# Kernel optimization log

Measured on AMD Instinct MI355X. Metric: run time of the kernel, lower is better.

Reference implementation:

```python
import jax, jax.numpy as jnp
import numpy as np

EPS = 0.1
P, C, T_MLP, C_MLP, B = 196, 768, 384, 3072, 64


def yat(x, W, b, alpha):
    # x: (..., in), W: (out, in), b: (out,), alpha: (1,)
    dot_nb = jnp.einsum('...i,oi->...o', x, W)          # no-bias dot (shared GEMM)
    dot = dot_nb + b
    w_norm_sq = jnp.sum(W * W, axis=1)                   # (out,)
    x_norm_sq = jnp.sum(x * x, axis=-1, keepdims=True)   # (..., 1)
    dist_sq = w_norm_sq + x_norm_sq - 2.0 * dot_nb
    out_f = W.shape[0]
    scale_base = out_f / np.log(out_f + 1.0)
    scale = jnp.sqrt(jnp.asarray(scale_base, x.dtype)) ** alpha[0]
    return scale * (dot * dot) / (dist_sq + EPS)


def setup_inputs() -> dict:
    key = jax.random.key(0)
    ks = jax.random.split(key, 7)
    x = jax.random.normal(ks[0], (B, P, C), dtype=jnp.float32)
    # token-mixing YAT: in=P, out=T_MLP
    tw = jax.random.normal(ks[1], (T_MLP, P), dtype=jnp.float32) / np.sqrt(P)
    tb = jnp.zeros((T_MLP,), jnp.float32)
    t_alpha = jnp.ones((1,), jnp.float32)
    # token-mixing linear: T_MLP -> P
    w2 = jax.random.uniform(ks[2], (P, T_MLP), jnp.float32, -1, 1) / np.sqrt(T_MLP)
    b2 = jax.random.uniform(ks[3], (P,), jnp.float32, -1, 1) / np.sqrt(T_MLP)
    # channel-mixing YAT: in=C, out=C_MLP
    cw = jax.random.normal(ks[4], (C_MLP, C), dtype=jnp.float32) / np.sqrt(C)
    cb = jnp.zeros((C_MLP,), jnp.float32)
    c_alpha = jnp.ones((1,), jnp.float32)
    # channel-mixing linear: C_MLP -> C
    w4 = jax.random.uniform(ks[5], (C, C_MLP), jnp.float32, -1, 1) / np.sqrt(C_MLP)
    b4 = jax.random.uniform(ks[6], (C,), jnp.float32, -1, 1) / np.sqrt(C_MLP)
    return {"x": x, "tw": tw, "tb": tb, "t_alpha": t_alpha, "w2": w2, "b2": b2,
            "cw": cw, "cb": cb, "c_alpha": c_alpha, "w4": w4, "b4": b4}


def reference(x, tw, tb, t_alpha, w2, b2, cw, cb, c_alpha, w4, b4):
    # Token mixing (operates over patch dim)
    shortcut = x
    xt = jnp.swapaxes(x, 1, 2)                 # (B, C, P)
    h = yat(xt, tw, tb, t_alpha)               # (B, C, T_MLP)
    h = jnp.einsum('bct,pt->bcp', h, w2) + b2  # (B, C, P)
    x = shortcut + jnp.swapaxes(h, 1, 2)
    # Channel mixing (operates over hidden dim)
    shortcut = x
    h = yat(x, cw, cb, c_alpha)                # (B, P, C_MLP)
    h = jnp.einsum('bpm,cm->bpc', h, w4) + b4  # (B, P, C)
    return shortcut + h
```

## Files before the change

### kernel.cpp

```cpp
#include <hip/hip_runtime.h>
#include <hip/hip_bf16.h>
#include <math.h>

#define B_   64
#define P_   196
#define PPAD 224
#define C_   768
#define TM_  384
#define CM_  3072
#define EPSY 0.1f

typedef unsigned short u16;
typedef __attribute__((ext_vector_type(8))) short bf16x8;
typedef __attribute__((ext_vector_type(4))) float f32x4;

__device__ __forceinline__ float bf2f(u16 v) {
    return __uint_as_float(((unsigned int)v) << 16);
}
__device__ __forceinline__ u16 f2bf(float f) {
    unsigned int u = __float_as_uint(f);
    unsigned int rounding = 0x7FFFu + ((u >> 16) & 1u);
    return (u16)((u + rounding) >> 16);
}

__device__ __forceinline__ void gl_lds16(const u16* g, u16* l) {
    __builtin_amdgcn_global_load_lds(
        (const __attribute__((address_space(1))) unsigned int*)g,
        (__attribute__((address_space(3))) unsigned int*)l,
        16, 0, 0);
}


__global__ __launch_bounds__(256) void k_prep_xT(const float* __restrict__ x,
                                                 u16* __restrict__ xT,
                                                 float* __restrict__ xn1) {
    __shared__ u16 tile[32][33];
    __shared__ float colsum[32];
    const int b = blockIdx.z, p0 = blockIdx.x * 32, c0 = blockIdx.y * 32;
    const int tx = threadIdx.x & 31, ty = threadIdx.x >> 5;
    if (threadIdx.x < 32) colsum[threadIdx.x] = 0.f;
    const float* xb = x + (size_t)b * P_ * C_;
    float s = 0.f;
    #pragma unroll
    for (int r = 0; r < 4; ++r) {
        int p = p0 + ty + r * 8;
        float v = (p < P_) ? xb[(size_t)p * C_ + c0 + tx] : 0.f;
        u16 h = f2bf(v);
        tile[ty + r * 8][tx] = h;
        float vb = bf2f(h);
        s = fmaf(vb, vb, s);
    }
    __syncthreads();
    u16* dst = xT + ((size_t)b * C_ + c0) * PPAD + p0;
    #pragma unroll
    for (int r = 0; r < 4; ++r) {
        int cl = ty + r * 8;
        dst[(size_t)cl * PPAD + tx] = tile[tx][cl];
    }
    atomicAdd(&colsum[tx], s);
    __syncthreads();
    if (threadIdx.x < 32)
        atomicAdd(&xn1[(size_t)b * C_ + c0 + threadIdx.x], colsum[threadIdx.x]);
}

__device__ __forceinline__ void pad_norm_body(const float* in, u16* outb, float* norm,
                                              int rows, int inlen, int outlen,
                                              int bid, int tid) {
    int wave = (bid * 256 + tid) >> 6;
    int lane = tid & 63;
    if (wave >= rows) return;
    const float* src = in + (size_t)wave * inlen;
    u16* dst = outb + (size_t)wave * outlen;
    float s = 0.f;
    for (int i = lane; i < outlen; i += 64) {
        float v = (i < inlen) ? src[i] : 0.f;
        u16 h = f2bf(v);
        dst[i] = h;
        float vv = bf2f(h);
        s = fmaf(vv, vv, s);
    }
    #pragma unroll
    for (int off = 32; off > 0; off >>= 1) s += __shfl_down(s, off, 64);
    if (lane == 0) norm[wave] = s;
}

__global__ __launch_bounds__(256) void k_prep_weights(
    const float* __restrict__ tw, u16* __restrict__ twb, float* __restrict__ twn,
    const float* __restrict__ cw, u16* __restrict__ cwb, float* __restrict__ cwn,
    const float* __restrict__ w2, u16* __restrict__ w2b,
    const float* __restrict__ w4, u16* __restrict__ w4b) {
    int bid = blockIdx.x, tid = threadIdx.x;
    if (bid < 96) {
        pad_norm_body(tw, twb, twn, TM_, P_, PPAD, bid, tid);
    } else if (bid < 864) {
        pad_norm_body(cw, cwb, cwn, CM_, C_, C_, bid - 96, tid);
    } else if (bid < 1248) {
        int idx = (bid - 864) * 256 + tid;
        int row = idx / TM_;
        w2b[idx] = (row < P_) ? f2bf(w2[(size_t)row * TM_ + (idx % TM_)]) : (u16)0;
    } else {
        int idx = (bid - 1248) * 256 + tid;
        float4 v = ((const float4*)w4)[idx];
        ushort4 o;
        o.x = f2bf(v.x); o.y = f2bf(v.y); o.z = f2bf(v.z); o.w = f2bf(v.w);
        ((ushort4*)w4b)[idx] = o;
    }
}

__device__ __forceinline__ void mfma_mainloop(
    const u16* __restrict__ A, const u16* __restrict__ B,
    int lda, int ldb, int kiters,
    f32x4 (&acc)[4][4], u16* As, u16* Bs) {
    const int t = threadIdx.x;
    const int w = t >> 6, l = t & 63;
    const int quad = l >> 4, l15 = l & 15;
    const int row0 = t >> 2, kc = (t & 3) * 8;

    const u16* pa0 = A + (size_t)row0 * lda + kc;
    const u16* pa1 = A + (size_t)(64 + row0) * lda + kc;
    const u16* pb0 = B + (size_t)row0 * ldb + kc;
    const u16* pb1 = B + (size_t)(64 + row0) * ldb + kc;

    u16* ldsA0 = As + w * 512;
    u16* ldsA1 = As + 2048 + w * 512;
    u16* ldsB0 = Bs + w * 512;
    u16* ldsB1 = Bs + 2048 + w * 512;

#define STAGE_(bsel, koff)                          \
    do {                                            \
        const int nb_ = (bsel) * 4096;              \
        gl_lds16(pa0 + (koff), ldsA0 + nb_);        \
        gl_lds16(pa1 + (koff), ldsA1 + nb_);        \
        gl_lds16(pb0 + (koff), ldsB0 + nb_);        \
        gl_lds16(pb1 + (koff), ldsB1 + nb_);        \
    } while (0)

    STAGE_(0, 0);
    if (kiters > 1) {
        STAGE_(1, 32);
        asm volatile("s_waitcnt vmcnt(4)" ::: "memory");
    } else {
        asm volatile("s_waitcnt vmcnt(0)" ::: "memory");
    }
    __builtin_amdgcn_s_barrier();

    int cur = 0;
    int koff = 64;
    for (int it = 0; it < kiters; ++it) {
        const u16* Aw = As + cur * 4096 + (w >> 1) * 2048;
        const u16* Bw = Bs + cur * 4096 + (w & 1) * 2048;
        bf16x8 af[4], bfr[4];
        #pragma unroll
        for (int i = 0; i < 4; ++i)
            af[i] = *(const bf16x8*)(Aw + ((i * 16 + l15) * 32 + quad * 8));
        #pragma unroll
        for (int j = 0; j < 4; ++j)
            bfr[j] = *(const bf16x8*)(Bw + ((j * 16 + l15) * 32 + quad * 8));
        asm volatile("s_waitcnt lgkmcnt(0)" ::: "memory");
        __builtin_amdgcn_sched_barrier(0);
        __builtin_amdgcn_s_barrier();
        const bool more2 = (it + 2 < kiters);
        if (more2) { STAGE_(cur, koff); koff += 32; }
        __builtin_amdgcn_s_setprio(1);
        #pragma unroll
        for (int i = 0; i < 4; ++i)
            #pragma unroll
            for (int j = 0; j < 4; ++j)
                acc[i][j] = __builtin_amdgcn_mfma_f32_16x16x32_bf16(af[i], bfr[j], acc[i][j], 0, 0, 0);
        __builtin_amdgcn_s_setprio(0);
        if (it + 1 < kiters) {
            if (more2) asm volatile("s_waitcnt vmcnt(4)" ::: "memory");
            else       asm volatile("s_waitcnt vmcnt(0)" ::: "memory");
            __builtin_amdgcn_s_barrier();
        }
        cur ^= 1;
    }
#undef STAGE_
}

#define MFMA_CORE(AP, BP, LDA, LDB, KITERS)                              \
    __shared__ u16 As[2 * 128 * 32];                                     \
    __shared__ u16 Bs[2 * 128 * 32];                                     \
    const int t = threadIdx.x;                                           \
    const int wid = t >> 6, lane = t & 63;                               \
    const int quad = lane >> 4, l15 = lane & 15;                         \
    f32x4 acc[4][4];                                                     \
    _Pragma("unroll")                                                    \
    for (int i = 0; i < 4; ++i)                                          \
        _Pragma("unroll")                                                \
        for (int j = 0; j < 4; ++j) acc[i][j] = (f32x4){0.f,0.f,0.f,0.f};\
    mfma_mainloop(AP, BP, LDA, LDB, KITERS, acc, As, Bs);                \
    const int rbase = m0 + (wid >> 1) * 64;                              \
    const int cbase = n0 + (wid & 1) * 64;

__global__ __launch_bounds__(256) void k1_token_yat(
    const u16* __restrict__ xT, const u16* __restrict__ twb,
    const float* __restrict__ tb, const float* __restrict__ twn,
    const float* __restrict__ xn1, const float* __restrict__ alpha, float sb,
    u16* __restrict__ h1) {
    const int m0 = (blockIdx.x + blockIdx.y * 8) * 128;
    const int n0 = blockIdx.z * 128;
    MFMA_CORE(xT + (size_t)m0 * PPAD, twb + (size_t)n0 * PPAD, PPAD, PPAD, PPAD / 32)
    float scale = powf(sqrtf(sb), alpha[0]);
    #pragma unroll
    for (int i = 0; i < 4; ++i) {
        #pragma unroll
        for (int j = 0; j < 4; ++j) {
            int col = cbase + j * 16 + l15;
            float bn = tb[col], wnn = twn[col];
            #pragma unroll
            for (int reg = 0; reg < 4; ++reg) {
                int row = rbase + i * 16 + quad * 4 + reg;
                float dnb = acc[i][j][reg];
                float dot = dnb + bn;
                float dist = wnn + xn1[row] - 2.f * dnb;
                h1[(size_t)row * TM_ + col] = f2bf(scale * dot * dot / (dist + EPSY));
            }
        }
    }
}

__global__ __launch_bounds__(256) void k3_chan_yat(
    const u16* __restrict__ x1b, const u16* __restrict__ cwb,
    const float* __restrict__ cb, const float* __restrict__ cwn,
    const float* __restrict__ xn2, const float* __restrict__ alpha, float sb,
    u16* __restrict__ h3) {
    const int mt = blockIdx.x + blockIdx.y * 8;
    if (mt >= B_ * P_ / 128) return;
    const int m0 = mt * 128;
    const int n0 = blockIdx.z * 128;
    MFMA_CORE(x1b + (size_t)m0 * C_, cwb + (size_t)n0 * C_, C_, C_, C_ / 32)
    float scale = powf(sqrtf(sb), alpha[0]);
    #pragma unroll
    for (int i = 0; i < 4; ++i) {
        #pragma unroll
        for (int j = 0; j < 4; ++j) {
            int col = cbase + j * 16 + l15;
            float bn = cb[col], wnn = cwn[col];
            #pragma unroll
            for (int reg = 0; reg < 4; ++reg) {
                int row = rbase + i * 16 + quad * 4 + reg;
                float dnb = acc[i][j][reg];
                float dot = dnb + bn;
                float dist = wnn + xn2[row] - 2.f * dnb;
                h3[(size_t)row * CM_ + col] = f2bf(scale * dot * dot / (dist + EPSY));
            }
        }
    }
}

__global__ __launch_bounds__(256) void k2_token_out(
    const u16* __restrict__ w2b, const u16* __restrict__ h1,
    const float* __restrict__ b2, const float* __restrict__ x,
    float* __restrict__ xn2, u16* __restrict__ x1b) {
    const int m0 = blockIdx.x * 128, n0 = blockIdx.y * 128;
    const u16* Bz = h1 + (size_t)blockIdx.z * C_ * TM_;
    MFMA_CORE(w2b + (size_t)m0 * TM_, Bz + (size_t)n0 * TM_, TM_, TM_, TM_ / 32)
    const float* rz = x + (size_t)blockIdx.z * P_ * C_;
    u16* oz = x1b + (size_t)blockIdx.z * P_ * C_;
    float* xrow = xn2 + (size_t)blockIdx.z * P_;
    #pragma unroll
    for (int i = 0; i < 4; ++i) {
        #pragma unroll
        for (int reg = 0; reg < 4; ++reg) {
            int row = rbase + i * 16 + quad * 4 + reg;
            if (row < P_) {
                float bm = b2[row];
                float s = 0.f;
                #pragma unroll
                for (int j = 0; j < 4; ++j) {
                    int col = cbase + j * 16 + l15;
                    float v = acc[i][j][reg] + bm + rz[(size_t)row * C_ + col];
                    u16 h = f2bf(v);
                    oz[(size_t)row * C_ + col] = h;
                    float vb = bf2f(h);
                    s = fmaf(vb, vb, s);
                }
                s += __shfl_xor(s, 1, 64);
                s += __shfl_xor(s, 2, 64);
                s += __shfl_xor(s, 4, 64);
                s += __shfl_xor(s, 8, 64);
                if (l15 == 0) atomicAdd(&xrow[row], s);
            }
        }
    }
}

__global__ __launch_bounds__(256) void k4_split(
    const u16* __restrict__ h3, const u16* __restrict__ w4b,
    u16* __restrict__ pbuf, int KK) {
    const int mt = blockIdx.x + blockIdx.y * 8;
    if (mt >= B_ * P_ / 128) return;
    const int m0 = mt * 128;
    const int nz = blockIdx.z;
    const int n0 = (nz % (C_ / 128)) * 128;
    const int ks = nz / (C_ / 128);
    const int kbase = ks * KK;
    MFMA_CORE(h3 + (size_t)m0 * CM_ + kbase, w4b + (size_t)n0 * CM_ + kbase,
              CM_, CM_, KK / 32)
    u16* dst = pbuf + (size_t)ks * ((size_t)B_ * P_ * C_);
    #pragma unroll
    for (int i = 0; i < 4; ++i) {
        #pragma unroll
        for (int j = 0; j < 4; ++j) {
            int col = cbase + j * 16 + l15;
            #pragma unroll
            for (int reg = 0; reg < 4; ++reg) {
                int row = rbase + i * 16 + quad * 4 + reg;
                dst[(size_t)row * C_ + col] = f2bf(acc[i][j][reg]);
            }
        }
    }
}

template <int NS>
__global__ __launch_bounds__(256) void k4_reduce(
    float* __restrict__ outp, const u16* __restrict__ pbuf,
    const u16* __restrict__ x1b, const float* __restrict__ b4) {
    int idx = blockIdx.x * 256 + threadIdx.x;
    int c = (idx * 4) % C_;
    ushort4 r = ((const ushort4*)x1b)[idx];
    float4 o;
    o.x = bf2f(r.x) + b4[c + 0];
    o.y = bf2f(r.y) + b4[c + 1];
    o.z = bf2f(r.z) + b4[c + 2];
    o.w = bf2f(r.w) + b4[c + 3];
    const size_t stride4 = (size_t)B_ * P_ * C_ / 4;
    #pragma unroll
    for (int s = 0; s < NS; ++s) {
        ushort4 p = ((const ushort4*)pbuf)[idx + s * stride4];
        o.x += bf2f(p.x); o.y += bf2f(p.y); o.z += bf2f(p.z); o.w += bf2f(p.w);
    }
    ((float4*)outp)[idx] = o;
}

__global__ __launch_bounds__(256) void gemm_k4_fb(
    const u16* __restrict__ A, const u16* __restrict__ Bmat,
    const float* __restrict__ biasN, const u16* __restrict__ resB,
    float* __restrict__ Fout) {
    __shared__ u16 As[128 * 32];
    __shared__ u16 Bs[64 * 32];
    const int t = threadIdx.x;
    const int wid = t >> 6, lane = t & 63;
    const int quad = lane >> 4, l15 = lane & 15;
    const int m0 = blockIdx.x * 128, n0 = blockIdx.y * 64;
    f32x4 acc[4][2];
    #pragma unroll
    for (int i = 0; i < 4; ++i)
        #pragma unroll
        for (int j = 0; j < 2; ++j) acc[i][j] = (f32x4){0.f, 0.f, 0.f, 0.f};
    const u16* Aw = As + (wid >> 1) * (64 * 32);
    const u16* Bw = Bs + (wid & 1) * (32 * 32);
    const int arow = t >> 2, akc = (t & 3) * 8;
    for (int k0 = 0; k0 < CM_; k0 += 32) {
        gl_lds16(A + (size_t)(m0 + arow) * CM_ + k0 + akc,      As + wid * 512);
        gl_lds16(A + (size_t)(m0 + 64 + arow) * CM_ + k0 + akc, As + 2048 + wid * 512);
        gl_lds16(Bmat + (size_t)(n0 + arow) * CM_ + k0 + akc,   Bs + wid * 512);
        __syncthreads();
        bf16x8 af[4], bfr[2];
        #pragma unroll
        for (int i = 0; i < 4; ++i)
            af[i] = *(const bf16x8*)(Aw + ((i * 16 + l15) * 32 + quad * 8));
        #pragma unroll
        for (int j = 0; j < 2; ++j)
            bfr[j] = *(const bf16x8*)(Bw + ((j * 16 + l15) * 32 + quad * 8));
        #pragma unroll
        for (int i = 0; i < 4; ++i)
            #pragma unroll
            for (int j = 0; j < 2; ++j)
                acc[i][j] = __builtin_amdgcn_mfma_f32_16x16x32_bf16(af[i], bfr[j], acc[i][j], 0, 0, 0);
        __syncthreads();
    }
    const int rbase = m0 + (wid >> 1) * 64;
    const int cbase = n0 + (wid & 1) * 32;
    #pragma unroll
    for (int i = 0; i < 4; ++i) {
        #pragma unroll
        for (int j = 0; j < 2; ++j) {
            int col = cbase + j * 16 + l15;
            float bn = biasN[col];
            #pragma unroll
            for (int reg = 0; reg < 4; ++reg) {
                int row = rbase + i * 16 + quad * 4 + reg;
                float v = acc[i][j][reg] + bn + bf2f(resB[(size_t)row * C_ + col]);
                Fout[(size_t)row * C_ + col] = v;
            }
        }
    }
}

extern "C" void kernel_launch(void* const* d_in, const int* in_sizes, int n_in,
                              void* d_out, int out_size, void* d_ws, size_t ws_size,
                              hipStream_t stream) {
    const float* x  = (const float*)d_in[0];
    const float* tw = (const float*)d_in[1];
    const float* tb = (const float*)d_in[2];
    const float* ta = (const float*)d_in[3];
    const float* w2 = (const float*)d_in[4];
    const float* b2 = (const float*)d_in[5];
    const float* cw = (const float*)d_in[6];
    const float* cb = (const float*)d_in[7];
    const float* ca = (const float*)d_in[8];
    const float* w4 = (const float*)d_in[9];
    const float* b4 = (const float*)d_in[10];
    float* out = (float*)d_out;

    char* ws = (char*)d_ws;
    u16* h1 = (u16*)ws;
    u16* xT = (u16*)(ws + 37748736);
    u16* h3 = (u16*)ws;
    size_t off = 77070336;
    u16* x1b = (u16*)(ws + off); off += (size_t)B_ * P_ * C_ * 2;
    u16* twb = (u16*)(ws + off); off += (size_t)TM_ * PPAD * 2;
    u16* w2b = (u16*)(ws + off); off += (size_t)256 * TM_ * 2;
    u16* cwb = (u16*)(ws + off); off += (size_t)CM_ * C_ * 2;
    u16* w4b = (u16*)(ws + off); off += (size_t)C_ * CM_ * 2;
    float* xn1 = (float*)(ws + off); off += (size_t)B_ * C_ * 4;
    float* xn2 = (float*)(ws + off); off += (size_t)B_ * P_ * 4;
    float* twn = (float*)(ws + off); off += (size_t)TM_ * 4;
    float* cwn = (float*)(ws + off); off += (size_t)CM_ * 4;
    u16* pbuf = (u16*)(ws + off);
    const size_t psz = (size_t)B_ * P_ * C_ * 2;

    int nsplit = 1;
    if (ws_size >= off + 4 * psz)      nsplit = 4;
    else if (ws_size >= off + 2 * psz) nsplit = 2;

    const float SBT = (float)TM_ / logf((float)TM_ + 1.0f);
    const float SBC = (float)CM_ / logf((float)CM_ + 1.0f);

    hipMemsetAsync(xn1, 0, (size_t)(B_ * C_ + B_ * P_) * 4, stream);
    k_prep_weights<<<3552, 256, 0, stream>>>(tw, twb, twn, cw, cwb, cwn,
                                             w2, w2b, w4, w4b);
    k_prep_xT<<<dim3(PPAD / 32, C_ / 32, B_), 256, 0, stream>>>(x, xT, xn1);

    k1_token_yat<<<dim3(8, 48, 3), 256, 0, stream>>>(
        xT, twb, tb, twn, xn1, ta, SBT, h1);

    k2_token_out<<<dim3(2, C_ / 128, B_), 256, 0, stream>>>(
        w2b, h1, b2, x, xn2, x1b);

    k3_chan_yat<<<dim3(8, 13, 24), 256, 0, stream>>>(
        x1b, cwb, cb, cwn, xn2, ca, SBC, h3);

    if (nsplit > 1) {
        k4_split<<<dim3(8, 13, (C_ / 128) * nsplit), 256, 0, stream>>>(
            h3, w4b, pbuf, CM_ / nsplit);
        int n4 = B_ * P_ * C_ / 4;
        if (nsplit == 4)
            k4_reduce<4><<<(n4 + 255) / 256, 256, 0, stream>>>(out, pbuf, x1b, b4);
        else
            k4_reduce<2><<<(n4 + 255) / 256, 256, 0, stream>>>(out, pbuf, x1b, b4);
    } else {
        gemm_k4_fb<<<dim3(B_ * P_ / 128, C_ / 64), 256, 0, stream>>>(
            h3, w4b, b4, x1b, out);
    }
}
```

Measured before the change: 385.5 us.

## Use 256x256 block tiles with 512 threads for channel GEMMs

Adds a new MFMA main loop that computes 256x256 output tiles with 8 waves, each wave holding a 128x64 accumulator, and switches the channel-mixing YAT and the split-K output GEMM to it. Larger tiles raise arithmetic intensity and cut global and LDS traffic per FLOP in the two largest GEMMs. In exchange each thread holds twice as many accumulator registers and there are fewer blocks. M=12544 is 49 tiles of 256, so the grid launches 56 tile slots and idles the extra 7.

```diff
diff --git a/kernel.cpp b/kernel.cpp
--- a/kernel.cpp
+++ b/kernel.cpp
@@ -193,6 +193,77 @@
     const int rbase = m0 + (wid >> 1) * 64;                              \
     const int cbase = n0 + (wid & 1) * 64;
 
+__device__ __forceinline__ void mfma256_mainloop(
+    const u16* __restrict__ A, const u16* __restrict__ B,
+    int lda, int ldb, int kiters,
+    f32x4 (&acc)[8][4], u16* smem,
+    int wr, int wc, int l15, int quad) {
+    const int t = threadIdx.x;
+    const int cxor = (quad * 8) ^ ((l15 & 3) * 8);
+
+    const int off0 = t * 8;
+    const int s0 = off0 ^ (((off0 >> 5) & 3) << 3);
+    const int gr0 = s0 >> 5, gc0 = s0 & 31;
+    const int off1 = 4096 + t * 8;
+    const int s1 = off1 ^ (((off1 >> 5) & 3) << 3);
+    const int gr1 = s1 >> 5, gc1 = s1 & 31;
+
+    const u16* a0 = A + (size_t)gr0 * lda + gc0;
+    const u16* a1 = A + (size_t)gr1 * lda + gc1;
+    const u16* b0 = B + (size_t)gr0 * ldb + gc0;
+    const u16* b1 = B + (size_t)gr1 * ldb + gc1;
+
+#define STG256_(d, k0)                                   \
+    do {                                                 \
+        u16* sb_ = smem + (d) * 8192;                    \
+        gl_lds16(a0 + (k0), sb_ + off0);                 \
+        gl_lds16(a1 + (k0), sb_ + off1);                 \
+        gl_lds16(b0 + (k0), sb_ + 16384 + off0);         \
+        gl_lds16(b1 + (k0), sb_ + 16384 + off1);         \
+    } while (0)
+
+    STG256_(0, 0);
+    if (kiters > 1) {
+        STG256_(1, 32);
+        asm volatile("s_waitcnt vmcnt(4)" ::: "memory");
+    } else {
+        asm volatile("s_waitcnt vmcnt(0)" ::: "memory");
+    }
+    __builtin_amdgcn_s_barrier();
+
+    int cur = 0;
+    for (int it = 0; it < kiters; ++it) {
+        const u16* Ab = smem + cur * 8192;
+        const u16* Bb = smem + 16384 + cur * 8192;
+        bf16x8 bfr[4];
+        #pragma unroll
+        for (int n = 0; n < 4; ++n)
+            bfr[n] = *(const bf16x8*)(Bb + (wc * 64 + n * 16 + l15) * 32 + cxor);
+        __builtin_amdgcn_s_setprio(1);
+        #pragma unroll
+        for (int m = 0; m < 8; ++m) {
+            bf16x8 af = *(const bf16x8*)(Ab + (wr * 128 + m * 16 + l15) * 32 + cxor);
+            #pragma unroll
+            for (int n = 0; n < 4; ++n)
+                acc[m][n] = __builtin_amdgcn_mfma_f32_16x16x32_bf16(af, bfr[n], acc[m][n], 0, 0, 0);
+        }
+        __builtin_amdgcn_s_setprio(0);
+        asm volatile("s_waitcnt lgkmcnt(0)" ::: "memory");
+        __builtin_amdgcn_sched_barrier(0);
+        __builtin_amdgcn_s_barrier();
+        if (it + 2 < kiters) {
+            STG256_(cur, (it + 2) * 32);
+            asm volatile("s_waitcnt vmcnt(4)" ::: "memory");
+            __builtin_amdgcn_s_barrier();
+        } else if (it + 1 < kiters) {
+            asm volatile("s_waitcnt vmcnt(0)" ::: "memory");
+            __builtin_amdgcn_s_barrier();
+        }
+        cur ^= 1;
+    }
+#undef STG256_
+}
+
 __global__ __launch_bounds__(256) void k1_token_yat(
     const u16* __restrict__ xT, const u16* __restrict__ twb,
     const float* __restrict__ tb, const float* __restrict__ twn,
@@ -220,27 +291,40 @@
     }
 }
 
-__global__ __launch_bounds__(256) void k3_chan_yat(
+__global__ __launch_bounds__(512) void k3_chan_yat(
     const u16* __restrict__ x1b, const u16* __restrict__ cwb,
     const float* __restrict__ cb, const float* __restrict__ cwn,
     const float* __restrict__ xn2, const float* __restrict__ alpha, float sb,
     u16* __restrict__ h3) {
+    __shared__ __align__(16) u16 smem[32768];
     const int mt = blockIdx.x + blockIdx.y * 8;
-    if (mt >= B_ * P_ / 128) return;
-    const int m0 = mt * 128;
-    const int n0 = blockIdx.z * 128;
-    MFMA_CORE(x1b + (size_t)m0 * C_, cwb + (size_t)n0 * C_, C_, C_, C_ / 32)
+    if (mt >= (B_ * P_) / 256) return;
+    const int m0 = mt * 256;
+    const int n0 = blockIdx.z * 256;
+    const int t = threadIdx.x;
+    const int wid = t >> 6, l = t & 63;
+    const int wr = wid >> 2, wc = wid & 3;
+    const int quad = l >> 4, l15 = l & 15;
+    f32x4 acc[8][4];
+    #pragma unroll
+    for (int m = 0; m < 8; ++m)
+        #pragma unroll
+        for (int n = 0; n < 4; ++n) acc[m][n] = (f32x4){0.f, 0.f, 0.f, 0.f};
+    mfma256_mainloop(x1b + (size_t)m0 * C_, cwb + (size_t)n0 * C_,
+                     C_, C_, C_ / 32, acc, smem, wr, wc, l15, quad);
+    const int rbase = m0 + wr * 128;
+    const int cbase = n0 + wc * 64;
     float scale = powf(sqrtf(sb), alpha[0]);
     #pragma unroll
-    for (int i = 0; i < 4; ++i) {
-        #pragma unroll
-        for (int j = 0; j < 4; ++j) {
-            int col = cbase + j * 16 + l15;
+    for (int m = 0; m < 8; ++m) {
+        #pragma unroll
+        for (int n = 0; n < 4; ++n) {
+            int col = cbase + n * 16 + l15;
             float bn = cb[col], wnn = cwn[col];
             #pragma unroll
             for (int reg = 0; reg < 4; ++reg) {
-                int row = rbase + i * 16 + quad * 4 + reg;
-                float dnb = acc[i][j][reg];
+                int row = rbase + m * 16 + quad * 4 + reg;
+                float dnb = acc[m][n][reg];
                 float dot = dnb + bn;
                 float dist = wnn + xn2[row] - 2.f * dnb;
                 h3[(size_t)row * CM_ + col] = f2bf(scale * dot * dot / (dist + EPSY));
@@ -286,28 +370,40 @@
     }
 }
 
-__global__ __launch_bounds__(256) void k4_split(
+__global__ __launch_bounds__(512) void k4_split(
     const u16* __restrict__ h3, const u16* __restrict__ w4b,
     u16* __restrict__ pbuf, int KK) {
+    __shared__ __align__(16) u16 smem[32768];
     const int mt = blockIdx.x + blockIdx.y * 8;
-    if (mt >= B_ * P_ / 128) return;
-    const int m0 = mt * 128;
+    if (mt >= (B_ * P_) / 256) return;
+    const int m0 = mt * 256;
     const int nz = blockIdx.z;
-    const int n0 = (nz % (C_ / 128)) * 128;
-    const int ks = nz / (C_ / 128);
+    const int n0 = (nz % 3) * 256;
+    const int ks = nz / 3;
     const int kbase = ks * KK;
-    MFMA_CORE(h3 + (size_t)m0 * CM_ + kbase, w4b + (size_t)n0 * CM_ + kbase,
-              CM_, CM_, KK / 32)
+    const int t = threadIdx.x;
+    const int wid = t >> 6, l = t & 63;
+    const int wr = wid >> 2, wc = wid & 3;
+    const int quad = l >> 4, l15 = l & 15;
+    f32x4 acc[8][4];
+    #pragma unroll
+    for (int m = 0; m < 8; ++m)
+        #pragma unroll
+        for (int n = 0; n < 4; ++n) acc[m][n] = (f32x4){0.f, 0.f, 0.f, 0.f};
+    mfma256_mainloop(h3 + (size_t)m0 * CM_ + kbase, w4b + (size_t)n0 * CM_ + kbase,
+                     CM_, CM_, KK / 32, acc, smem, wr, wc, l15, quad);
+    const int rbase = m0 + wr * 128;
+    const int cbase = n0 + wc * 64;
     u16* dst = pbuf + (size_t)ks * ((size_t)B_ * P_ * C_);
     #pragma unroll
-    for (int i = 0; i < 4; ++i) {
-        #pragma unroll
-        for (int j = 0; j < 4; ++j) {
-            int col = cbase + j * 16 + l15;
+    for (int m = 0; m < 8; ++m) {
+        #pragma unroll
+        for (int n = 0; n < 4; ++n) {
+            int col = cbase + n * 16 + l15;
             #pragma unroll
             for (int reg = 0; reg < 4; ++reg) {
-                int row = rbase + i * 16 + quad * 4 + reg;
-                dst[(size_t)row * C_ + col] = f2bf(acc[i][j][reg]);
+                int row = rbase + m * 16 + quad * 4 + reg;
+                dst[(size_t)row * C_ + col] = f2bf(acc[m][n][reg]);
             }
         }
     }
@@ -440,11 +536,11 @@
     k2_token_out<<<dim3(2, C_ / 128, B_), 256, 0, stream>>>(
         w2b, h1, b2, x, xn2, x1b);
 
-    k3_chan_yat<<<dim3(8, 13, 24), 256, 0, stream>>>(
+    k3_chan_yat<<<dim3(8, 7, 12), 512, 0, stream>>>(
         x1b, cwb, cb, cwn, xn2, ca, SBC, h3);
 
     if (nsplit > 1) {
-        k4_split<<<dim3(8, 13, (C_ / 128) * nsplit), 256, 0, stream>>>(
+        k4_split<<<dim3(8, 7, 3 * nsplit), 512, 0, stream>>>(
             h3, w4b, pbuf, CM_ / nsplit);
         int n4 = B_ * P_ * C_ / 4;
         if (nsplit == 4)
```

New measurement: 420.1 us. +9.0%, slower.
